# Kernel optimization log

Measured on AMD Instinct MI355X. Metric: run time of the kernel, lower is better.

Reference implementation:

```python
import jax, jax.numpy as jnp
import numpy as np

C = 768
NUM_HEADS = 12
HEAD_DIM = C // NUM_HEADS
AGENT_NUM = 49
POOL = 7  # sqrt(agent_num)
EPS = 1e-5


def _with_bias_ln(x, w, b):
    # LayerNorm over last dim, biased variance, eps=1e-5
    mu = x.mean(-1, keepdims=True)
    var = ((x - mu) ** 2).mean(-1, keepdims=True)
    return (x - mu) / jnp.sqrt(var + EPS) * w + b


def setup_inputs() -> dict:
    key = jax.random.key(0)
    ks = jax.random.split(key, 8)
    B, H, W = 8, 56, 56
    inp = {
        "x": jax.random.normal(ks[0], (B, C, H, W), dtype=jnp.float32),
        "y": jax.random.normal(ks[1], (B, C, H, W), dtype=jnp.float32),
        "ln1_w": jnp.ones((C,), jnp.float32),
        "ln1_b": jnp.zeros((C,), jnp.float32),
        "ln2_w": jnp.ones((C,), jnp.float32),
        "ln2_b": jnp.zeros((C,), jnp.float32),
        # torch nn.Linear weight layout: [out, in]
        "wq1": jax.random.normal(ks[2], (C, C), jnp.float32) * 0.02,
        "wq2": jax.random.normal(ks[3], (C, C), jnp.float32) * 0.02,
        "wkv": jax.random.normal(ks[4], (2 * C, C), jnp.float32) * 0.02,
        "wproj": jax.random.normal(ks[5], (C, C), jnp.float32) * 0.02,
        "bproj": jnp.zeros((C,), jnp.float32),
    }
    return inp


def reference(x, y, ln1_w, ln1_b, ln2_w, ln2_b, wq1, wq2, wkv, wproj, bproj):
    b, c, h, w = x.shape
    n = h * w
    nh, hd = NUM_HEADS, HEAD_DIM
    scale = hd ** (-0.5)

    # NCHW -> (b, n, c) token layout
    xt = x.reshape(b, c, n).transpose(0, 2, 1)
    yt = y.reshape(b, c, n).transpose(0, 2, 1)

    xt = _with_bias_ln(xt, ln1_w, ln1_b)
    yt = _with_bias_ln(yt, ln2_w, ln2_b)

    q = jnp.einsum('bnc,oc->bno', xt, wq1)        # (b, n, c)
    q_agent = jnp.einsum('bnc,oc->bno', yt, wq2)  # (b, n, c)
    kv = jnp.einsum('bnc,oc->bno', xt, wkv)       # (b, n, 2c)
    k, v = kv[..., :c], kv[..., c:]

    # Adaptive avg pool q_agent to 7x7 agent tokens (56/7 = 8 exact windows)
    qa = q_agent.reshape(b, h, w, c)
    qa = qa.reshape(b, POOL, h // POOL, POOL, w // POOL, c).mean(axis=(2, 4))
    agent_tokens = qa.reshape(b, AGENT_NUM, c)

    # split heads: (b, heads, tokens, head_dim)
    q = q.reshape(b, n, nh, hd).transpose(0, 2, 1, 3)
    k = k.reshape(b, n, nh, hd).transpose(0, 2, 1, 3)
    v = v.reshape(b, n, nh, hd).transpose(0, 2, 1, 3)
    at = agent_tokens.reshape(b, AGENT_NUM, nh, hd).transpose(0, 2, 1, 3)

    # stage 1: agent tokens attend over keys -> pooled values
    agent_attn = jax.nn.softmax(jnp.einsum('bhad,bhnd->bhan', at * scale, k), axis=-1)
    agent_v = jnp.einsum('bhan,bhnd->bhad', agent_attn, v)  # (b, h, A, hd)

    # stage 2: queries attend over agent tokens
    q_attn = jax.nn.softmax(jnp.einsum('bhnd,bhad->bhna', q * scale, at), axis=-1)
    out = jnp.einsum('bhna,bhad->bhnd', q_attn, agent_v)  # (b, h, n, hd)

    out = out.transpose(0, 2, 1, 3).reshape(b, n, c)
    out = jnp.einsum('bnc,oc->bno', out, wproj) + bproj
    return out.transpose(0, 2, 1).reshape(b, c, h, w)
```

## Files before the change

### kernel.cpp

```cpp
#include <hip/hip_runtime.h>

typedef unsigned short u16;
typedef u16 u16x4 __attribute__((ext_vector_type(4)));
typedef u16 u16x8 __attribute__((ext_vector_type(8)));
typedef __bf16 bf16x8 __attribute__((ext_vector_type(8)));
typedef float f32x4 __attribute__((ext_vector_type(4)));

__device__ __forceinline__ float b2f(u16 u) {
    union { unsigned int i; float f; } v; v.i = ((unsigned int)u) << 16; return v.f;
}
__device__ __forceinline__ u16 f2b(float f) {
    union { float f; unsigned int i; } v; v.f = f;
    unsigned int r = v.i + 0x7fffu + ((v.i >> 16) & 1u);
    return (u16)(r >> 16);
}
__device__ __forceinline__ void gload_lds16(const u16* g, u16* l) {
    __builtin_amdgcn_global_load_lds(
        (const __attribute__((address_space(1))) void*)g,
        (__attribute__((address_space(3))) void*)l, 16, 0, 0);
}
__device__ __forceinline__ bf16x8 ones_frag() {
    union { u16x8 u; bf16x8 b; } v;
    #pragma unroll
    for (int i = 0; i < 8; ++i) v.u[i] = 0x3F80;
    return v.b;
}
#define LGKM_BARRIER do { \
    asm volatile("s_waitcnt lgkmcnt(0)" ::: "memory"); \
    __builtin_amdgcn_s_barrier(); \
    __builtin_amdgcn_sched_barrier(0); } while (0)

__global__ __launch_bounds__(256) void pack_w_kernel(
    const float* __restrict__ wq1, const float* __restrict__ wq2,
    const float* __restrict__ wkv, const float* __restrict__ wproj,
    u16* __restrict__ wcat, u16* __restrict__ wq2b, u16* __restrict__ wpb,
    u16* __restrict__ at_a) {
    int e = blockIdx.x * 256 + threadIdx.x;
    const float scale = 0.125f;
    wcat[e]           = f2b(wq1[e] * scale);
    wcat[589824 + e]  = f2b(wkv[e] * scale);
    wcat[1179648 + e] = f2b(wkv[589824 + e]);
    wq2b[e]           = f2b(wq2[e]);
    wpb[e]            = f2b(wproj[e]);
    if (e < 92160) {
        int bb = e / 11520, rem = e - bb * 11520;
        at_a[(size_t)bb * 49152 + 37632 + rem] = 0;
    }
}

__global__ __launch_bounds__(256) void ln_x_kernel(
    const float* __restrict__ x, const float* __restrict__ lw,
    const float* __restrict__ lb, u16* __restrict__ xn) {
    __shared__ float red[16][64];
    __shared__ float red2[16][64];
    __shared__ float smu[64];
    __shared__ float srs[64];
    __shared__ u16 tl[128][68];
    const int bx = blockIdx.x;
    const int b = bx / 49, tile = bx - b * 49;
    const int pos0 = tile * 64;
    const int t = threadIdx.x;
    const int pq = t & 15, q = t >> 4;
    const float* xb = x + (size_t)b * 2408448 + pos0;

    f32x4 s = {0.f, 0.f, 0.f, 0.f}, s2 = {0.f, 0.f, 0.f, 0.f};
    #pragma unroll 8
    for (int c = q; c < 768; c += 16) {
        f32x4 v = *(const f32x4*)&xb[(size_t)c * 3136 + pq * 4];
        s += v; s2 += v * v;
    }
    *(f32x4*)&red[q][pq * 4] = s;
    *(f32x4*)&red2[q][pq * 4] = s2;
    __syncthreads();
    if (t < 64) {
        float ss = 0.f, qq = 0.f;
        #pragma unroll
        for (int r = 0; r < 16; ++r) { ss += red[r][t]; qq += red2[r][t]; }
        float mu = ss * (1.0f / 768.0f);
        float var = qq * (1.0f / 768.0f) - mu * mu;
        smu[t] = mu;
        srs[t] = rsqrtf(var + 1e-5f);
    }
    __syncthreads();

    const int p = t >> 2, sub = t & 3;
    const size_t orow = ((size_t)(b * 3136 + pos0 + p)) * 768;
    for (int c0 = 0; c0 < 768; c0 += 128) {
        #pragma unroll
        for (int s8 = 0; s8 < 8; ++s8) {
            const int cr = s8 * 16 + q;
            f32x4 v = *(const f32x4*)&xb[(size_t)(c0 + cr) * 3136 + pq * 4];
            u16x4 pk;
            pk[0] = f2b(v[0]); pk[1] = f2b(v[1]); pk[2] = f2b(v[2]); pk[3] = f2b(v[3]);
            *(u16x4*)&tl[cr][pq * 4] = pk;
        }
        __syncthreads();
        const float mu = smu[p], rs = srs[p];
        #pragma unroll
        for (int k = 0; k < 4; ++k) {
            const int cb = k * 32 + sub * 8;
            f32x4 w0 = *(const f32x4*)&lw[c0 + cb];
            f32x4 w1 = *(const f32x4*)&lw[c0 + cb + 4];
            f32x4 b0 = *(const f32x4*)&lb[c0 + cb];
            f32x4 b1 = *(const f32x4*)&lb[c0 + cb + 4];
            u16x8 o;
            #pragma unroll
            for (int j = 0; j < 4; ++j) {
                float v = b2f(tl[cb + j][p]);
                o[j] = f2b((v - mu) * rs * w0[j] + b0[j]);
            }
            #pragma unroll
            for (int j = 0; j < 4; ++j) {
                float v = b2f(tl[cb + 4 + j][p]);
                o[4 + j] = f2b((v - mu) * rs * w1[j] + b1[j]);
            }
            *(u16x8*)&xn[orow + c0 + cb] = o;
        }
        __syncthreads();
    }
}

__global__ __launch_bounds__(256) void y_stats_kernel(
    const float* __restrict__ y, float* __restrict__ rsb, float* __restrict__ mrsb) {
    __shared__ float red[16][64];
    __shared__ float red2[16][64];
    const int bx = blockIdx.x;
    const int b = bx / 49, tile = bx - b * 49;
    const int pos0 = tile * 64;
    const int t = threadIdx.x, pq = t & 15, q = t >> 4;
    const float* yb = y + (size_t)b * 2408448 + pos0;
    f32x4 s = {0.f, 0.f, 0.f, 0.f}, s2 = {0.f, 0.f, 0.f, 0.f};
    #pragma unroll 8
    for (int c = q; c < 768; c += 16) {
        f32x4 v = *(const f32x4*)&yb[(size_t)c * 3136 + pq * 4];
        s += v; s2 += v * v;
    }
    *(f32x4*)&red[q][pq * 4] = s;
    *(f32x4*)&red2[q][pq * 4] = s2;
    __syncthreads();
    if (t < 64) {
        float ss = 0.f, qq = 0.f;
        #pragma unroll
        for (int r = 0; r < 16; ++r) { ss += red[r][t]; qq += red2[r][t]; }
        float mu = ss * (1.0f / 768.0f);
        float var = qq * (1.0f / 768.0f) - mu * mu;
        float rv = rsqrtf(var + 1e-5f);
        rsb[(size_t)b * 3136 + pos0 + t] = rv;
        mrsb[(size_t)b * 3136 + pos0 + t] = mu * rv;
    }
}

__global__ __launch_bounds__(256) void y_pool_kernel(
    const float* __restrict__ y, const float* __restrict__ lw,
    const float* __restrict__ lb, const float* __restrict__ rsb,
    const float* __restrict__ mrsb, u16* __restrict__ at_a) {
    const int cgrp = blockIdx.x;
    const int bpi  = blockIdx.y;
    const int b = bpi / 7, pi = bpi - b * 7;
    const int t = threadIdx.x, lane = t & 63, w = t >> 6;
    const int pbase = b * 3136 + pi * 448;
    const int p0 = (lane >> 3) * 56 + (lane & 7);
    float rsv[7], s3f[7];
    #pragma unroll
    for (int it = 0; it < 7; ++it) {
        rsv[it] = rsb[pbase + p0 + it * 8];
        float m = mrsb[pbase + p0 + it * 8];
        #pragma unroll
        for (int msk = 1; msk < 64; msk <<= 1) m += __shfl_xor(m, msk, 64);
        s3f[it] = m;
    }
    const float* yb = y + (size_t)b * 2408448 + pi * 448 + p0;
    u16* yo = at_a + ((size_t)b * 64 + pi * 7) * 768;
    for (int ci = 0; ci < 16; ++ci) {
        const int c = cgrp * 64 + w * 16 + ci;
        const float* yc = yb + (size_t)c * 3136;
        float v[7];
        #pragma unroll
        for (int it = 0; it < 7; ++it) v[it] = yc[it * 8] * rsv[it];
        #pragma unroll
        for (int it = 0; it < 7; ++it) {
            float s = v[it];
            #pragma unroll
            for (int msk = 1; msk < 64; msk <<= 1) s += __shfl_xor(s, msk, 64);
            v[it] = s;
        }
        if (lane == 0) {
            const float wv = lw[c], bv = lb[c];
            #pragma unroll
            for (int it = 0; it < 7; ++it)
                yo[(size_t)it * 768 + c] = f2b(wv * (v[it] - s3f[it]) * (1.0f / 64.0f) + bv);
        }
    }
}

template<int MODE, int NCT>
__global__ __launch_bounds__(256) void gemm_bt_kernel(
    const u16* __restrict__ A, const u16* __restrict__ B,
    u16* __restrict__ qk, u16* __restrict__ vT,
    float* __restrict__ Cf, const float* __restrict__ bias) {
    __shared__ u16 As[128 * 64];
    __shared__ u16 Bs[128 * 64];
    const int t = threadIdx.x;
    const int lane = t & 63;
    const int w = t >> 6;
    const int wr = w >> 1, wc = w & 1;
    const int l15 = lane & 15, l4 = lane >> 4;

    const int nwg = gridDim.x;
    const int orig = blockIdx.x;
    const int xcd = orig & 7;
    const int qd = nwg >> 3, r = nwg & 7;
    const int wg = (xcd < r ? xcd * (qd + 1) : r * (qd + 1) + (xcd - r) * qd) + (orig >> 3);
    const int ct = wg % NCT, rt = wg / NCT;

    const u16* Ab = A + (size_t)rt * 128 * 768;
    const u16* Bb = B + (size_t)ct * 128 * 768;
    const int grh = lane >> 3;
    const int gsl = (lane & 7) ^ grh;

    f32x4 acc[4][4];
    #pragma unroll
    for (int mi = 0; mi < 4; ++mi)
        #pragma unroll
        for (int ni = 0; ni < 4; ++ni)
            acc[mi][ni] = (f32x4){0.f, 0.f, 0.f, 0.f};

    for (int kt = 0; kt < 12; ++kt) {
        if (kt) __syncthreads();
        #pragma unroll
        for (int i = 0; i < 4; ++i) {
            const int chunk = w * 4 + i;
            const int row = chunk * 8 + grh;
            gload_lds16(Ab + (size_t)row * 768 + kt * 64 + gsl * 8, &As[chunk * 512]);
            gload_lds16(Bb + (size_t)row * 768 + kt * 64 + gsl * 8, &Bs[chunk * 512]);
        }
        __syncthreads();
        #pragma unroll
        for (int ks = 0; ks < 2; ++ks) {
            bf16x8 af[4], bfv[4];
            #pragma unroll
            for (int mi = 0; mi < 4; ++mi) {
                const int row = wr * 64 + mi * 16 + l15;
                af[mi] = *(const bf16x8*)&As[row * 64 + (((ks * 4 + l4) ^ (row & 7)) * 8)];
            }
            #pragma unroll
            for (int ni = 0; ni < 4; ++ni) {
                const int row = wc * 64 + ni * 16 + l15;
                bfv[ni] = *(const bf16x8*)&Bs[row * 64 + (((ks * 4 + l4) ^ (row & 7)) * 8)];
            }
            #pragma unroll
            for (int mi = 0; mi < 4; ++mi)
                #pragma unroll
                for (int ni = 0; ni < 4; ++ni)
                    acc[mi][ni] = __builtin_amdgcn_mfma_f32_16x16x32_bf16(
                        af[mi], bfv[ni], acc[mi][ni], 0, 0, 0);
        }
    }

    if constexpr (MODE == 0) {
        #pragma unroll
        for (int mi = 0; mi < 4; ++mi)
            #pragma unroll
            for (int ni = 0; ni < 4; ++ni) {
                const int row0 = rt * 128 + wr * 64 + mi * 16 + l4 * 4;
                const int col = ct * 128 + wc * 64 + ni * 16 + l15;
                if (col < 1536) {
                    #pragma unroll
                    for (int rr = 0; rr < 4; ++rr)
                        qk[(size_t)(row0 + rr) * 1536 + col] = f2b(acc[mi][ni][rr]);
                } else {
                    const int c = col - 1536;
                    const int bb = row0 / 3136;
                    const int nn2 = row0 - bb * 3136;
                    u16x4 pk;
                    #pragma unroll
                    for (int rr = 0; rr < 4; ++rr) pk[rr] = f2b(acc[mi][ni][rr]);
                    *(u16x4*)&vT[((size_t)(bb * 768 + c)) * 3136 + nn2] = pk;
                }
            }
    } else if constexpr (MODE == 1) {
        #pragma unroll
        for (int ni = 0; ni < 4; ++ni) {
            const int col = ct * 128 + wc * 64 + ni * 16 + l15;
            const float bv = bias[col];
            #pragma unroll
            for (int mi = 0; mi < 4; ++mi) {
                const int grow = rt * 128 + wr * 64 + mi * 16 + l4 * 4;
                const int bb = grow / 3136;
                const int nn2 = grow - bb * 3136;
                f32x4 vv = acc[mi][ni];
                vv[0] += bv; vv[1] += bv; vv[2] += bv; vv[3] += bv;
                *(f32x4*)(Cf + (size_t)bb * 2408448 + (size_t)col * 3136 + nn2) = vv;
            }
        }
    } else {
        #pragma unroll
        for (int mi = 0; mi < 4; ++mi)
            #pragma unroll
            for (int ni = 0; ni < 4; ++ni) {
                const int row0 = rt * 128 + wr * 64 + mi * 16 + l4 * 4;
                const int col = ct * 128 + wc * 64 + ni * 16 + l15;
                #pragma unroll
                for (int rr = 0; rr < 4; ++rr)
                    qk[(size_t)(row0 + rr) * 768 + col] = f2b(acc[mi][ni][rr]);
            }
    }
}

__global__ __launch_bounds__(256) void agent_attn_kernel(
    const u16* __restrict__ at_bf, const u16* __restrict__ qk,
    const u16* __restrict__ vT, float* __restrict__ ps,
    float* __restrict__ pav_t) {
    __shared__ u16 k_lds[2][64 * 64];
    __shared__ u16 vt_lds[2][64 * 64];
    __shared__ u16 p_lds[64 * 64];
    const int ns = blockIdx.x;
    const int bh = blockIdx.y;
    const int b = bh / 12, h = bh - b * 12;
    const int t = threadIdx.x, lane = t & 63, w = t >> 6;
    const int l15 = lane & 15, l4 = lane >> 4;

    bf16x8 atf[2];
    #pragma unroll
    for (int ks = 0; ks < 2; ++ks)
        atf[ks] = *(const bf16x8*)&at_bf[((size_t)b * 64 + 16 * w + l15) * 768 + h * 64 + ks * 32 + l4 * 8];
    const bf16x8 onef = ones_frag();

    f32x4 acc_o[4], acc_den[4];
    #pragma unroll
    for (int mi = 0; mi < 4; ++mi) {
        acc_o[mi] = (f32x4){0.f, 0.f, 0.f, 0.f};
        acc_den[mi] = (f32x4){0.f, 0.f, 0.f, 0.f};
    }

    auto STAGE = [&](int buf, int tile) {
        const int n0 = ns * 448 + tile * 64;
        #pragma unroll
        for (int p = 0; p < 2; ++p) {
            const int row = p * 32 + w * 8 + (lane >> 3);
            const int sc = ((lane & 7) ^ (row & 7)) * 8;
            gload_lds16(qk + ((size_t)(b * 3136 + n0 + row)) * 1536 + 768 + h * 64 + sc,
                        &k_lds[buf][(p * 32 + w * 8) * 64]);
            gload_lds16(vT + ((size_t)(bh * 64 + row)) * 3136 + n0 + sc,
                        &vt_lds[buf][(p * 32 + w * 8) * 64]);
        }
    };

    STAGE(0, 0);
    for (int tile = 0; tile < 7; ++tile) {
        const int buf = tile & 1;
        __syncthreads();
        if (tile < 6) STAGE(buf ^ 1, tile + 1);
        f32x4 acc_s[4];
        #pragma unroll
        for (int mi = 0; mi < 4; ++mi) acc_s[mi] = (f32x4){0.f, 0.f, 0.f, 0.f};
        #pragma unroll
        for (int ks = 0; ks < 2; ++ks)
            #pragma unroll
            for (int mi = 0; mi < 4; ++mi) {
                const int row = 16 * mi + l15;
                bf16x8 kf = *(const bf16x8*)&k_lds[buf][row * 64 + (((ks * 4 + l4) ^ (row & 7)) * 8)];
                acc_s[mi] = __builtin_amdgcn_mfma_f32_16x16x32_bf16(kf, atf[ks], acc_s[mi], 0, 0, 0);
            }
        const int a_w = 16 * w + l15;
        #pragma unroll
        for (int mi = 0; mi < 4; ++mi) {
            u16x4 pk;
            #pragma unroll
            for (int rr = 0; rr < 4; ++rr) pk[rr] = f2b(__expf(acc_s[mi][rr]));
            const int pp = (2 * mi + (l4 >> 1)) ^ (a_w & 7);
            *(u16x4*)((char*)p_lds + a_w * 128 + pp * 16 + (l4 & 1) * 8) = pk;
        }
        LGKM_BARRIER;
        #pragma unroll
        for (int ks = 0; ks < 2; ++ks) {
            const int d = 16 * w + l15;
            bf16x8 vf = *(const bf16x8*)&vt_lds[buf][d * 64 + (((ks * 4 + l4) ^ (d & 7)) * 8)];
            #pragma unroll
            for (int mi = 0; mi < 4; ++mi) {
                const int a = 16 * mi + l15;
                bf16x8 pf = *(const bf16x8*)((char*)p_lds + a * 128 + (((ks * 4 + l4) ^ (a & 7)) * 16));
                acc_o[mi] = __builtin_amdgcn_mfma_f32_16x16x32_bf16(pf, vf, acc_o[mi], 0, 0, 0);
                acc_den[mi] = __builtin_amdgcn_mfma_f32_16x16x32_bf16(onef, pf, acc_den[mi], 0, 0, 0);
            }
        }
    }
    const size_t pbase = (size_t)bh * 7 + ns;
    if (w == 0 && lane < 16) {
        #pragma unroll
        for (int mi = 0; mi < 4; ++mi)
            ps[pbase * 64 + 16 * mi + lane] = acc_den[mi][0];
    }
    #pragma unroll
    for (int mi = 0; mi < 4; ++mi)
        *(f32x4*)&pav_t[(pbase * 64 + 16 * w + l15) * 64 + 16 * mi + l4 * 4] = acc_o[mi];
}

__global__ __launch_bounds__(256) void combine_kernel(
    const float* __restrict__ ps, const float* __restrict__ pav_t,
    u16* __restrict__ av_t) {
    __shared__ float sinv[64];
    const int bh = blockIdx.x;
    const int t = threadIdx.x;
    if (t < 64) {
        float s = 0.f;
        #pragma unroll
        for (int ns = 0; ns < 7; ++ns) s += ps[((size_t)bh * 7 + ns) * 64 + t];
        sinv[t] = 1.0f / s;
    }
    __syncthreads();
    const int d = t >> 2, aseg = t & 3;
    f32x4 acc[4];
    #pragma unroll
    for (int g = 0; g < 4; ++g) acc[g] = (f32x4){0.f, 0.f, 0.f, 0.f};
    #pragma unroll
    for (int ns = 0; ns < 7; ++ns) {
        const float* src = pav_t + (((size_t)bh * 7 + ns) * 64 + d) * 64 + aseg * 16;
        #pragma unroll
        for (int g = 0; g < 4; ++g) acc[g] += *(const f32x4*)&src[g * 4];
    }
    u16x8 o0, o1;
    #pragma unroll
    for (int g = 0; g < 4; ++g)
        #pragma unroll
        for (int j = 0; j < 4; ++j) {
            const u16 v = f2b(acc[g][j] * sinv[aseg * 16 + g * 4 + j]);
            if (g < 2) o0[g * 4 + j] = v; else o1[(g - 2) * 4 + j] = v;
        }
    u16* dst = av_t + ((size_t)bh * 64 + d) * 64 + aseg * 16;
    *(u16x8*)dst = o0;
    *(u16x8*)(dst + 8) = o1;
}

__global__ __launch_bounds__(256) void q_attn_kernel(
    const u16* __restrict__ at_bf, const u16* __restrict__ qk,
    const u16* __restrict__ av_t, u16* __restrict__ attn_out) {
    __shared__ u16 q_lds[2][64 * 64];
    __shared__ u16 p_lds[64 * 64];
    const int grp = blockIdx.x;
    const int bh = blockIdx.y;
    const int b = bh / 12, h = bh - b * 12;
    const int t = threadIdx.x, lane = t & 63, w = t >> 6;
    const int l15 = lane & 15, l4 = lane >> 4;

    bf16x8 atf[4][2], avf[4][2];
    #pragma unroll
    for (int mi = 0; mi < 4; ++mi)
        #pragma unroll
        for (int ks = 0; ks < 2; ++ks) {
            atf[mi][ks] = *(const bf16x8*)&at_bf[((size_t)b * 64 + 16 * mi + l15) * 768 + h * 64 + ks * 32 + l4 * 8];
            avf[mi][ks] = *(const bf16x8*)&av_t[((size_t)bh * 64 + 16 * mi + l15) * 64 + ks * 32 + l4 * 8];
        }
    const bf16x8 onef = ones_frag();

    auto STAGE_Q = [&](int buf, int nt) {
        const int n0 = nt * 64;
        #pragma unroll
        for (int p = 0; p < 2; ++p) {
            const int row = p * 32 + w * 8 + (lane >> 3);
            const int sc = ((lane & 7) ^ (row & 7)) * 8;
            gload_lds16(qk + ((size_t)(b * 3136 + n0 + row)) * 1536 + h * 64 + sc,
                        &q_lds[buf][(p * 32 + w * 8) * 64]);
        }
    };

    STAGE_Q(0, grp * 7);
    const int nn = 16 * w + l15;
    for (int i = 0; i < 7; ++i) {
        const int buf = i & 1;
        const int nt = grp * 7 + i;
        __syncthreads();
        if (i < 6) STAGE_Q(buf ^ 1, nt + 1);
        f32x4 acc_l[4];
        #pragma unroll
        for (int mi = 0; mi < 4; ++mi) acc_l[mi] = (f32x4){0.f, 0.f, 0.f, 0.f};
        #pragma unroll
        for (int ks = 0; ks < 2; ++ks) {
            bf16x8 qf = *(const bf16x8*)&q_lds[buf][nn * 64 + (((ks * 4 + l4) ^ (nn & 7)) * 8)];
            #pragma unroll
            for (int mi = 0; mi < 4; ++mi)
                acc_l[mi] = __builtin_amdgcn_mfma_f32_16x16x32_bf16(atf[mi][ks], qf, acc_l[mi], 0, 0, 0);
        }
        #pragma unroll
        for (int mi = 0; mi < 4; ++mi) {
            u16x4 pk;
            #pragma unroll
            for (int rr = 0; rr < 4; ++rr) {
                const int a = 16 * mi + l4 * 4 + rr;
                pk[rr] = (a < 49) ? f2b(__expf(acc_l[mi][rr])) : (u16)0;
            }
            const int pp = (2 * mi + (l4 >> 1)) ^ (nn & 7);
            *(u16x4*)((char*)p_lds + nn * 128 + pp * 16 + (l4 & 1) * 8) = pk;
        }
        LGKM_BARRIER;
        f32x4 acc_o[4], den;
        #pragma unroll
        for (int mi = 0; mi < 4; ++mi) acc_o[mi] = (f32x4){0.f, 0.f, 0.f, 0.f};
        den = (f32x4){0.f, 0.f, 0.f, 0.f};
        #pragma unroll
        for (int ks = 0; ks < 2; ++ks) {
            bf16x8 pf = *(const bf16x8*)((char*)p_lds + nn * 128 + (((ks * 4 + l4) ^ (nn & 7)) * 16));
            den = __builtin_amdgcn_mfma_f32_16x16x32_bf16(onef, pf, den, 0, 0, 0);
            #pragma unroll
            for (int mi = 0; mi < 4; ++mi)
                acc_o[mi] = __builtin_amdgcn_mfma_f32_16x16x32_bf16(avf[mi][ks], pf, acc_o[mi], 0, 0, 0);
        }
        const float rinv = 1.0f / den[0];
        const size_t obase = ((size_t)(b * 3136 + nt * 64 + nn)) * 768 + h * 64;
        #pragma unroll
        for (int mi = 0; mi < 4; ++mi) {
            u16x4 ov;
            #pragma unroll
            for (int rr = 0; rr < 4; ++rr) ov[rr] = f2b(acc_o[mi][rr] * rinv);
            *(u16x4*)&attn_out[obase + 16 * mi + l4 * 4] = ov;
        }
    }
}

extern "C" void kernel_launch(void* const* d_in, const int* in_sizes, int n_in,
                              void* d_out, int out_size, void* d_ws, size_t ws_size,
                              hipStream_t stream) {
    (void)in_sizes; (void)n_in; (void)out_size; (void)ws_size;
    const float* x     = (const float*)d_in[0];
    const float* y     = (const float*)d_in[1];
    const float* ln1w  = (const float*)d_in[2];
    const float* ln1b  = (const float*)d_in[3];
    const float* ln2w  = (const float*)d_in[4];
    const float* ln2b  = (const float*)d_in[5];
    const float* wq1   = (const float*)d_in[6];
    const float* wq2   = (const float*)d_in[7];
    const float* wkv   = (const float*)d_in[8];
    const float* wproj = (const float*)d_in[9];
    const float* bproj = (const float*)d_in[10];
    float* out = (float*)d_out;

    char* ws = (char*)d_ws;
    u16*   xn     = (u16*)(ws);
    u16*   qk     = (u16*)(ws + 38535168);
    u16*   vT     = (u16*)(ws + 115605504);
    u16*   wcat   = (u16*)(ws + 154140672);
    u16*   wq2b   = (u16*)(ws + 157679616);
    u16*   wpb    = (u16*)(ws + 158859264);
    u16*   at_a   = (u16*)(ws + 160038912);
    u16*   at_bf  = (u16*)(ws + 160825344);
    float* ps     = (float*)(ws + 161611776);
    float* rsb    = (float*)(ws + 161783808);
    float* mrsb   = (float*)(ws + 161884160);
    u16*   av_t   = (u16*)(ws + 161984512);
    float* pav_t  = (float*)(ws);
    u16*   attn_out = xn;

    pack_w_kernel<<<dim3(2304), dim3(256), 0, stream>>>(wq1, wq2, wkv, wproj, wcat, wq2b, wpb, at_a);
    ln_x_kernel<<<dim3(392), dim3(256), 0, stream>>>(x, ln1w, ln1b, xn);
    y_stats_kernel<<<dim3(392), dim3(256), 0, stream>>>(y, rsb, mrsb);
    y_pool_kernel<<<dim3(12, 56), dim3(256), 0, stream>>>(y, ln2w, ln2b, rsb, mrsb, at_a);
    gemm_bt_kernel<0, 18><<<dim3(3528), dim3(256), 0, stream>>>(xn, wcat, qk, vT, nullptr, nullptr);
    gemm_bt_kernel<2, 6><<<dim3(24), dim3(256), 0, stream>>>(at_a, wq2b, at_bf, nullptr, nullptr, nullptr);
    agent_attn_kernel<<<dim3(7, 96), dim3(256), 0, stream>>>(at_bf, qk, vT, ps, pav_t);
    combine_kernel<<<dim3(96), dim3(256), 0, stream>>>(ps, pav_t, av_t);
    q_attn_kernel<<<dim3(7, 96), dim3(256), 0, stream>>>(at_bf, qk, av_t, attn_out);
    gemm_bt_kernel<1, 6><<<dim3(1176), dim3(256), 0, stream>>>(attn_out, wpb, nullptr, nullptr, out, bproj);
}
```

Baseline: 319.5 us.

## Use 256x256 double-buffered GEMM tiles for QKV and projection GEMMs

Replaces the 128x128 single-buffered GEMM with a 256x256 tile, 512-thread kernel that double-buffers LDS and prefetches the next K-tile while computing the current one. It uses explicit vmcnt waits, barriers and setprio around the MFMA bursts. The goal is more reuse per loaded byte and hiding global load latency in the large QKV and projection GEMMs. The small agent-token GEMM moves to a separate 128-tile kernel. The cost is 128KB of LDS per block, which lowers occupancy, and fewer workgroups for the projection GEMM (294 blocks).

```diff
diff --git a/kernel.cpp b/kernel.cpp
--- a/kernel.cpp
+++ b/kernel.cpp
@@ -194,16 +194,17 @@
 }
 
 template<int MODE, int NCT>
-__global__ __launch_bounds__(256) void gemm_bt_kernel(
+__global__ __launch_bounds__(512, 2) void gemm256_kernel(
     const u16* __restrict__ A, const u16* __restrict__ B,
     u16* __restrict__ qk, u16* __restrict__ vT,
     float* __restrict__ Cf, const float* __restrict__ bias) {
-    __shared__ u16 As[128 * 64];
-    __shared__ u16 Bs[128 * 64];
+    __shared__ u16 As[2][256 * 64];
+    __shared__ u16 Bs[2][256 * 64];
     const int t = threadIdx.x;
     const int lane = t & 63;
     const int w = t >> 6;
-    const int wr = w >> 1, wc = w & 1;
+    const int wr = w >> 2;
+    const int wc = w & 3;
     const int l15 = lane & 15, l4 = lane >> 4;
 
     const int nwg = gridDim.x;
@@ -213,57 +214,80 @@
     const int wg = (xcd < r ? xcd * (qd + 1) : r * (qd + 1) + (xcd - r) * qd) + (orig >> 3);
     const int ct = wg % NCT, rt = wg / NCT;
 
-    const u16* Ab = A + (size_t)rt * 128 * 768;
-    const u16* Bb = B + (size_t)ct * 128 * 768;
-    const int grh = lane >> 3;
-    const int gsl = (lane & 7) ^ grh;
-
-    f32x4 acc[4][4];
-    #pragma unroll
-    for (int mi = 0; mi < 4; ++mi)
+    const u16* Ab = A + (size_t)rt * 256 * 768;
+    const u16* Bb = B + (size_t)ct * 256 * 768;
+    const int gsl = (lane & 7) ^ (lane >> 3);
+
+    f32x4 acc[8][4];
+    #pragma unroll
+    for (int mi = 0; mi < 8; ++mi)
         #pragma unroll
         for (int ni = 0; ni < 4; ++ni)
             acc[mi][ni] = (f32x4){0.f, 0.f, 0.f, 0.f};
 
+    auto ISSUE = [&](int buf, int kt) {
+        const size_t go = (size_t)(w * 8 + (lane >> 3)) * 768 + (size_t)kt * 64 + gsl * 8;
+        #pragma unroll
+        for (int i = 0; i < 4; ++i) {
+            gload_lds16(Ab + go + (size_t)i * 49152, &As[buf][(i * 64 + w * 8) * 64]);
+            gload_lds16(Bb + go + (size_t)i * 49152, &Bs[buf][(i * 64 + w * 8) * 64]);
+        }
+    };
+
+    ISSUE(0, 0);
     for (int kt = 0; kt < 12; ++kt) {
-        if (kt) __syncthreads();
-        #pragma unroll
-        for (int i = 0; i < 4; ++i) {
-            const int chunk = w * 4 + i;
-            const int row = chunk * 8 + grh;
-            gload_lds16(Ab + (size_t)row * 768 + kt * 64 + gsl * 8, &As[chunk * 512]);
-            gload_lds16(Bb + (size_t)row * 768 + kt * 64 + gsl * 8, &Bs[chunk * 512]);
-        }
-        __syncthreads();
-        #pragma unroll
-        for (int ks = 0; ks < 2; ++ks) {
-            bf16x8 af[4], bfv[4];
-            #pragma unroll
-            for (int mi = 0; mi < 4; ++mi) {
-                const int row = wr * 64 + mi * 16 + l15;
-                af[mi] = *(const bf16x8*)&As[row * 64 + (((ks * 4 + l4) ^ (row & 7)) * 8)];
-            }
+        const int buf = kt & 1;
+        if (kt < 11) {
+            ISSUE(buf ^ 1, kt + 1);
+            asm volatile("s_waitcnt vmcnt(8)" ::: "memory");
+        } else {
+            asm volatile("s_waitcnt vmcnt(0)" ::: "memory");
+        }
+        __builtin_amdgcn_sched_barrier(0);
+        __builtin_amdgcn_s_barrier();
+        __builtin_amdgcn_sched_barrier(0);
+        const u16* as_ = &As[buf][0];
+        const u16* bs_ = &Bs[buf][0];
+        #pragma unroll
+        for (int p = 0; p < 4; ++p) {
+            const int mh = p >> 1, nh = p & 1;
+            bf16x8 af[4][2], bfv[2][2];
+            #pragma unroll
+            for (int ks = 0; ks < 2; ++ks) {
+                const int sw = ((ks * 4 + l4) ^ (l15 & 7)) * 8;
+                #pragma unroll
+                for (int mi = 0; mi < 4; ++mi)
+                    af[mi][ks] = *(const bf16x8*)&as_[(wr * 128 + mh * 64 + mi * 16 + l15) * 64 + sw];
+                #pragma unroll
+                for (int ni = 0; ni < 2; ++ni)
+                    bfv[ni][ks] = *(const bf16x8*)&bs_[(wc * 64 + nh * 32 + ni * 16 + l15) * 64 + sw];
+            }
+            __builtin_amdgcn_s_barrier();
+            asm volatile("s_waitcnt lgkmcnt(0)" ::: "memory");
+            __builtin_amdgcn_sched_barrier(0);
+            __builtin_amdgcn_s_setprio(1);
+            #pragma unroll
+            for (int ks = 0; ks < 2; ++ks)
+                #pragma unroll
+                for (int mi = 0; mi < 4; ++mi)
+                    #pragma unroll
+                    for (int ni = 0; ni < 2; ++ni)
+                        acc[mh * 4 + mi][nh * 2 + ni] = __builtin_amdgcn_mfma_f32_16x16x32_bf16(
+                            af[mi][ks], bfv[ni][ks], acc[mh * 4 + mi][nh * 2 + ni], 0, 0, 0);
+            __builtin_amdgcn_s_setprio(0);
+            __builtin_amdgcn_sched_barrier(0);
+            __builtin_amdgcn_s_barrier();
+            __builtin_amdgcn_sched_barrier(0);
+        }
+    }
+
+    if constexpr (MODE == 0) {
+        #pragma unroll
+        for (int mi = 0; mi < 8; ++mi)
             #pragma unroll
             for (int ni = 0; ni < 4; ++ni) {
-                const int row = wc * 64 + ni * 16 + l15;
-                bfv[ni] = *(const bf16x8*)&Bs[row * 64 + (((ks * 4 + l4) ^ (row & 7)) * 8)];
-            }
-            #pragma unroll
-            for (int mi = 0; mi < 4; ++mi)
-                #pragma unroll
-                for (int ni = 0; ni < 4; ++ni)
-                    acc[mi][ni] = __builtin_amdgcn_mfma_f32_16x16x32_bf16(
-                        af[mi], bfv[ni], acc[mi][ni], 0, 0, 0);
-        }
-    }
-
-    if constexpr (MODE == 0) {
-        #pragma unroll
-        for (int mi = 0; mi < 4; ++mi)
-            #pragma unroll
-            for (int ni = 0; ni < 4; ++ni) {
-                const int row0 = rt * 128 + wr * 64 + mi * 16 + l4 * 4;
-                const int col = ct * 128 + wc * 64 + ni * 16 + l15;
+                const int row0 = rt * 256 + wr * 128 + mi * 16 + l4 * 4;
+                const int col = ct * 256 + wc * 64 + ni * 16 + l15;
                 if (col < 1536) {
                     #pragma unroll
                     for (int rr = 0; rr < 4; ++rr)
@@ -278,14 +302,14 @@
                     *(u16x4*)&vT[((size_t)(bb * 768 + c)) * 3136 + nn2] = pk;
                 }
             }
-    } else if constexpr (MODE == 1) {
+    } else {
         #pragma unroll
         for (int ni = 0; ni < 4; ++ni) {
-            const int col = ct * 128 + wc * 64 + ni * 16 + l15;
+            const int col = ct * 256 + wc * 64 + ni * 16 + l15;
             const float bv = bias[col];
             #pragma unroll
-            for (int mi = 0; mi < 4; ++mi) {
-                const int grow = rt * 128 + wr * 64 + mi * 16 + l4 * 4;
+            for (int mi = 0; mi < 8; ++mi) {
+                const int grow = rt * 256 + wr * 128 + mi * 16 + l4 * 4;
                 const int bb = grow / 3136;
                 const int nn2 = grow - bb * 3136;
                 f32x4 vv = acc[mi][ni];
@@ -293,18 +317,74 @@
                 *(f32x4*)(Cf + (size_t)bb * 2408448 + (size_t)col * 3136 + nn2) = vv;
             }
         }
-    } else {
-        #pragma unroll
-        for (int mi = 0; mi < 4; ++mi)
+    }
+}
+
+template<int NCT>
+__global__ __launch_bounds__(256) void gemm128_kernel(
+    const u16* __restrict__ A, const u16* __restrict__ B, u16* __restrict__ C) {
+    __shared__ u16 As[128 * 64];
+    __shared__ u16 Bs[128 * 64];
+    const int t = threadIdx.x;
+    const int lane = t & 63;
+    const int w = t >> 6;
+    const int wr = w >> 1, wc = w & 1;
+    const int l15 = lane & 15, l4 = lane >> 4;
+    const int ct = blockIdx.x % NCT, rt = blockIdx.x / NCT;
+
+    const u16* Ab = A + (size_t)rt * 128 * 768;
+    const u16* Bb = B + (size_t)ct * 128 * 768;
+    const int grh = lane >> 3;
+    const int gsl = (lane & 7) ^ grh;
+
+    f32x4 acc[4][4];
+    #pragma unroll
+    for (int mi = 0; mi < 4; ++mi)
+        #pragma unroll
+        for (int ni = 0; ni < 4; ++ni)
+            acc[mi][ni] = (f32x4){0.f, 0.f, 0.f, 0.f};
+
+    for (int kt = 0; kt < 12; ++kt) {
+        if (kt) __syncthreads();
+        #pragma unroll
+        for (int i = 0; i < 4; ++i) {
+            const int chunk = w * 4 + i;
+            const int row = chunk * 8 + grh;
+            gload_lds16(Ab + (size_t)row * 768 + kt * 64 + gsl * 8, &As[chunk * 512]);
+            gload_lds16(Bb + (size_t)row * 768 + kt * 64 + gsl * 8, &Bs[chunk * 512]);
+        }
+        __syncthreads();
+        #pragma unroll
+        for (int ks = 0; ks < 2; ++ks) {
+            bf16x8 af[4], bfv[4];
+            #pragma unroll
+            for (int mi = 0; mi < 4; ++mi) {
+                const int row = wr * 64 + mi * 16 + l15;
+                af[mi] = *(const bf16x8*)&As[row * 64 + (((ks * 4 + l4) ^ (row & 7)) * 8)];
+            }
             #pragma unroll
             for (int ni = 0; ni < 4; ++ni) {
-                const int row0 = rt * 128 + wr * 64 + mi * 16 + l4 * 4;
-                const int col = ct * 128 + wc * 64 + ni * 16 + l15;
+                const int row = wc * 64 + ni * 16 + l15;
+                bfv[ni] = *(const bf16x8*)&Bs[row * 64 + (((ks * 4 + l4) ^ (row & 7)) * 8)];
+            }
+            #pragma unroll
+            for (int mi = 0; mi < 4; ++mi)
                 #pragma unroll
-                for (int rr = 0; rr < 4; ++rr)
-                    qk[(size_t)(row0 + rr) * 768 + col] = f2b(acc[mi][ni][rr]);
-            }
-    }
+                for (int ni = 0; ni < 4; ++ni)
+                    acc[mi][ni] = __builtin_amdgcn_mfma_f32_16x16x32_bf16(
+                        af[mi], bfv[ni], acc[mi][ni], 0, 0, 0);
+        }
+    }
+    #pragma unroll
+    for (int mi = 0; mi < 4; ++mi)
+        #pragma unroll
+        for (int ni = 0; ni < 4; ++ni) {
+            const int row0 = rt * 128 + wr * 64 + mi * 16 + l4 * 4;
+            const int col = ct * 128 + wc * 64 + ni * 16 + l15;
+            #pragma unroll
+            for (int rr = 0; rr < 4; ++rr)
+                C[(size_t)(row0 + rr) * 768 + col] = f2b(acc[mi][ni][rr]);
+        }
 }
 
 __global__ __launch_bounds__(256) void agent_attn_kernel(
@@ -554,10 +634,10 @@
     ln_x_kernel<<<dim3(392), dim3(256), 0, stream>>>(x, ln1w, ln1b, xn);
     y_stats_kernel<<<dim3(392), dim3(256), 0, stream>>>(y, rsb, mrsb);
     y_pool_kernel<<<dim3(12, 56), dim3(256), 0, stream>>>(y, ln2w, ln2b, rsb, mrsb, at_a);
-    gemm_bt_kernel<0, 18><<<dim3(3528), dim3(256), 0, stream>>>(xn, wcat, qk, vT, nullptr, nullptr);
-    gemm_bt_kernel<2, 6><<<dim3(24), dim3(256), 0, stream>>>(at_a, wq2b, at_bf, nullptr, nullptr, nullptr);
+    gemm256_kernel<0, 9><<<dim3(882), dim3(512), 0, stream>>>(xn, wcat, qk, vT, nullptr, nullptr);
+    gemm128_kernel<6><<<dim3(24), dim3(256), 0, stream>>>(at_a, wq2b, at_bf);
     agent_attn_kernel<<<dim3(7, 96), dim3(256), 0, stream>>>(at_bf, qk, vT, ps, pav_t);
     combine_kernel<<<dim3(96), dim3(256), 0, stream>>>(ps, pav_t, av_t);
     q_attn_kernel<<<dim3(7, 96), dim3(256), 0, stream>>>(at_bf, qk, av_t, attn_out);
-    gemm_bt_kernel<1, 6><<<dim3(1176), dim3(256), 0, stream>>>(attn_out, wpb, nullptr, nullptr, out, bproj);
-}
+    gemm256_kernel<1, 3><<<dim3(294), dim3(512), 0, stream>>>(attn_out, wpb, nullptr, nullptr, out, bproj);
+}
```

Result: slower. 393.6 us (+23.2%).

## Merge launches: fuse pack+stats, norm+pool, QKV+agent GEMMs, combine into q_attn

Applied to the files above, without the earlier changes.

Reduces the launch count from ten to six. Weight packing is merged with the x/y LayerNorm statistics, x normalization (now split into two channel halves) is merged with y pooling, and the agent-token GEMM runs inside the QKV GEMM grid. The combine step is folded into q_attn, which rebuilds av_t in LDS in every block. GEMM tiles are also remapped into groups of 4 row tiles for L2 reuse. The cost is that the combine work is repeated 7 times per head and x is read twice (once for stats, once for normalization), but launch gaps and some serialization go away.

```diff
diff --git a/kernel.cpp b/kernel.cpp
--- a/kernel.cpp
+++ b/kernel.cpp
@@ -30,43 +30,43 @@
     __builtin_amdgcn_s_barrier(); \
     __builtin_amdgcn_sched_barrier(0); } while (0)
 
-__global__ __launch_bounds__(256) void pack_w_kernel(
+__global__ __launch_bounds__(256) void pack_stats_kernel(
     const float* __restrict__ wq1, const float* __restrict__ wq2,
     const float* __restrict__ wkv, const float* __restrict__ wproj,
     u16* __restrict__ wcat, u16* __restrict__ wq2b, u16* __restrict__ wpb,
-    u16* __restrict__ at_a) {
-    int e = blockIdx.x * 256 + threadIdx.x;
-    const float scale = 0.125f;
-    wcat[e]           = f2b(wq1[e] * scale);
-    wcat[589824 + e]  = f2b(wkv[e] * scale);
-    wcat[1179648 + e] = f2b(wkv[589824 + e]);
-    wq2b[e]           = f2b(wq2[e]);
-    wpb[e]            = f2b(wproj[e]);
-    if (e < 92160) {
-        int bb = e / 11520, rem = e - bb * 11520;
-        at_a[(size_t)bb * 49152 + 37632 + rem] = 0;
-    }
-}
-
-__global__ __launch_bounds__(256) void ln_x_kernel(
-    const float* __restrict__ x, const float* __restrict__ lw,
-    const float* __restrict__ lb, u16* __restrict__ xn) {
+    u16* __restrict__ at_a,
+    const float* __restrict__ x, const float* __restrict__ y,
+    float* __restrict__ xmu, float* __restrict__ xrs,
+    float* __restrict__ rsb, float* __restrict__ mrsb) {
     __shared__ float red[16][64];
     __shared__ float red2[16][64];
-    __shared__ float smu[64];
-    __shared__ float srs[64];
-    __shared__ u16 tl[128][68];
-    const int bx = blockIdx.x;
+    const int bxg = blockIdx.x;
+    const int t = threadIdx.x;
+    if (bxg < 2304) {
+        const int e = bxg * 256 + t;
+        const float scale = 0.125f;
+        wcat[e]           = f2b(wq1[e] * scale);
+        wcat[589824 + e]  = f2b(wkv[e] * scale);
+        wcat[1179648 + e] = f2b(wkv[589824 + e]);
+        wq2b[e]           = f2b(wq2[e]);
+        wpb[e]            = f2b(wproj[e]);
+        if (e < 92160) {
+            int bb = e / 11520, rem = e - bb * 11520;
+            at_a[(size_t)bb * 49152 + 37632 + rem] = 0;
+        }
+        return;
+    }
+    const int bx0 = bxg - 2304;
+    const int isY = bx0 >= 392;
+    const int bx = isY ? bx0 - 392 : bx0;
     const int b = bx / 49, tile = bx - b * 49;
     const int pos0 = tile * 64;
-    const int t = threadIdx.x;
     const int pq = t & 15, q = t >> 4;
-    const float* xb = x + (size_t)b * 2408448 + pos0;
-
+    const float* src = (isY ? y : x) + (size_t)b * 2408448 + pos0;
     f32x4 s = {0.f, 0.f, 0.f, 0.f}, s2 = {0.f, 0.f, 0.f, 0.f};
     #pragma unroll 8
     for (int c = q; c < 768; c += 16) {
-        f32x4 v = *(const f32x4*)&xb[(size_t)c * 3136 + pq * 4];
+        f32x4 v = *(const f32x4*)&src[(size_t)c * 3136 + pq * 4];
         s += v; s2 += v * v;
     }
     *(f32x4*)&red[q][pq * 4] = s;
@@ -78,86 +78,74 @@
         for (int r = 0; r < 16; ++r) { ss += red[r][t]; qq += red2[r][t]; }
         float mu = ss * (1.0f / 768.0f);
         float var = qq * (1.0f / 768.0f) - mu * mu;
-        smu[t] = mu;
-        srs[t] = rsqrtf(var + 1e-5f);
-    }
-    __syncthreads();
-
-    const int p = t >> 2, sub = t & 3;
-    const size_t orow = ((size_t)(b * 3136 + pos0 + p)) * 768;
-    for (int c0 = 0; c0 < 768; c0 += 128) {
-        #pragma unroll
-        for (int s8 = 0; s8 < 8; ++s8) {
-            const int cr = s8 * 16 + q;
-            f32x4 v = *(const f32x4*)&xb[(size_t)(c0 + cr) * 3136 + pq * 4];
-            u16x4 pk;
-            pk[0] = f2b(v[0]); pk[1] = f2b(v[1]); pk[2] = f2b(v[2]); pk[3] = f2b(v[3]);
-            *(u16x4*)&tl[cr][pq * 4] = pk;
-        }
-        __syncthreads();
-        const float mu = smu[p], rs = srs[p];
-        #pragma unroll
-        for (int k = 0; k < 4; ++k) {
-            const int cb = k * 32 + sub * 8;
-            f32x4 w0 = *(const f32x4*)&lw[c0 + cb];
-            f32x4 w1 = *(const f32x4*)&lw[c0 + cb + 4];
-            f32x4 b0 = *(const f32x4*)&lb[c0 + cb];
-            f32x4 b1 = *(const f32x4*)&lb[c0 + cb + 4];
-            u16x8 o;
-            #pragma unroll
-            for (int j = 0; j < 4; ++j) {
-                float v = b2f(tl[cb + j][p]);
-                o[j] = f2b((v - mu) * rs * w0[j] + b0[j]);
-            }
-            #pragma unroll
-            for (int j = 0; j < 4; ++j) {
-                float v = b2f(tl[cb + 4 + j][p]);
-                o[4 + j] = f2b((v - mu) * rs * w1[j] + b1[j]);
-            }
-            *(u16x8*)&xn[orow + c0 + cb] = o;
-        }
-        __syncthreads();
-    }
-}
-
-__global__ __launch_bounds__(256) void y_stats_kernel(
-    const float* __restrict__ y, float* __restrict__ rsb, float* __restrict__ mrsb) {
-    __shared__ float red[16][64];
-    __shared__ float red2[16][64];
-    const int bx = blockIdx.x;
-    const int b = bx / 49, tile = bx - b * 49;
-    const int pos0 = tile * 64;
-    const int t = threadIdx.x, pq = t & 15, q = t >> 4;
-    const float* yb = y + (size_t)b * 2408448 + pos0;
-    f32x4 s = {0.f, 0.f, 0.f, 0.f}, s2 = {0.f, 0.f, 0.f, 0.f};
-    #pragma unroll 8
-    for (int c = q; c < 768; c += 16) {
-        f32x4 v = *(const f32x4*)&yb[(size_t)c * 3136 + pq * 4];
-        s += v; s2 += v * v;
-    }
-    *(f32x4*)&red[q][pq * 4] = s;
-    *(f32x4*)&red2[q][pq * 4] = s2;
-    __syncthreads();
-    if (t < 64) {
-        float ss = 0.f, qq = 0.f;
-        #pragma unroll
-        for (int r = 0; r < 16; ++r) { ss += red[r][t]; qq += red2[r][t]; }
-        float mu = ss * (1.0f / 768.0f);
-        float var = qq * (1.0f / 768.0f) - mu * mu;
         float rv = rsqrtf(var + 1e-5f);
-        rsb[(size_t)b * 3136 + pos0 + t] = rv;
-        mrsb[(size_t)b * 3136 + pos0 + t] = mu * rv;
-    }
-}
-
-__global__ __launch_bounds__(256) void y_pool_kernel(
-    const float* __restrict__ y, const float* __restrict__ lw,
-    const float* __restrict__ lb, const float* __restrict__ rsb,
+        const size_t o = (size_t)b * 3136 + pos0 + t;
+        if (isY) { rsb[o] = rv; mrsb[o] = mu * rv; }
+        else     { xmu[o] = mu; xrs[o] = rv; }
+    }
+}
+
+__global__ __launch_bounds__(256) void norm_pool_kernel(
+    const float* __restrict__ x, const float* __restrict__ lw1,
+    const float* __restrict__ lb1, const float* __restrict__ xmu,
+    const float* __restrict__ xrs, u16* __restrict__ xn,
+    const float* __restrict__ y, const float* __restrict__ lw2,
+    const float* __restrict__ lb2, const float* __restrict__ rsb,
     const float* __restrict__ mrsb, u16* __restrict__ at_a) {
-    const int cgrp = blockIdx.x;
-    const int bpi  = blockIdx.y;
+    __shared__ u16 tl[128][68];
+    const int bxg = blockIdx.x;
+    const int t = threadIdx.x;
+    if (bxg < 784) {
+        const int half = bxg / 392;
+        const int bx = bxg - half * 392;
+        const int b = bx / 49, tile = bx - b * 49;
+        const int pos0 = tile * 64;
+        const int pq = t & 15, q = t >> 4;
+        const int p = t >> 2, sub = t & 3;
+        const float* xb = x + (size_t)b * 2408448 + pos0;
+        const float mu = xmu[(size_t)b * 3136 + pos0 + p];
+        const float rs = xrs[(size_t)b * 3136 + pos0 + p];
+        const size_t orow = ((size_t)(b * 3136 + pos0 + p)) * 768;
+        for (int ci = 0; ci < 3; ++ci) {
+            const int c0 = half * 384 + ci * 128;
+            #pragma unroll
+            for (int s8 = 0; s8 < 8; ++s8) {
+                const int cr = s8 * 16 + q;
+                f32x4 v = *(const f32x4*)&xb[(size_t)(c0 + cr) * 3136 + pq * 4];
+                u16x4 pk;
+                pk[0] = f2b(v[0]); pk[1] = f2b(v[1]); pk[2] = f2b(v[2]); pk[3] = f2b(v[3]);
+                *(u16x4*)&tl[cr][pq * 4] = pk;
+            }
+            __syncthreads();
+            #pragma unroll
+            for (int k = 0; k < 4; ++k) {
+                const int cb = k * 32 + sub * 8;
+                f32x4 w0 = *(const f32x4*)&lw1[c0 + cb];
+                f32x4 w1 = *(const f32x4*)&lw1[c0 + cb + 4];
+                f32x4 b0 = *(const f32x4*)&lb1[c0 + cb];
+                f32x4 b1 = *(const f32x4*)&lb1[c0 + cb + 4];
+                u16x8 o;
+                #pragma unroll
+                for (int j = 0; j < 4; ++j) {
+                    float v = b2f(tl[cb + j][p]);
+                    o[j] = f2b((v - mu) * rs * w0[j] + b0[j]);
+                }
+                #pragma unroll
+                for (int j = 0; j < 4; ++j) {
+                    float v = b2f(tl[cb + 4 + j][p]);
+                    o[4 + j] = f2b((v - mu) * rs * w1[j] + b1[j]);
+                }
+                *(u16x8*)&xn[orow + c0 + cb] = o;
+            }
+            __syncthreads();
+        }
+        return;
+    }
+    const int j = bxg - 784;
+    const int cgrp = j % 12;
+    const int bpi = j / 12;
     const int b = bpi / 7, pi = bpi - b * 7;
-    const int t = threadIdx.x, lane = t & 63, w = t >> 6;
+    const int lane = t & 63, w = t >> 6;
     const int pbase = b * 3136 + pi * 448;
     const int p0 = (lane >> 3) * 56 + (lane & 7);
     float rsv[7], s3f[7];
@@ -185,7 +173,7 @@
             v[it] = s;
         }
         if (lane == 0) {
-            const float wv = lw[c], bv = lb[c];
+            const float wv = lw2[c], bv = lb2[c];
             #pragma unroll
             for (int it = 0; it < 7; ++it)
                 yo[(size_t)it * 768 + c] = f2b(wv * (v[it] - s3f[it]) * (1.0f / 64.0f) + bv);
@@ -193,25 +181,17 @@
     }
 }
 
-template<int MODE, int NCT>
-__global__ __launch_bounds__(256) void gemm_bt_kernel(
-    const u16* __restrict__ A, const u16* __restrict__ B,
+template<int MODE>
+__device__ __forceinline__ void gemm_body(
+    int rt, int ct, const u16* __restrict__ A, const u16* __restrict__ B,
     u16* __restrict__ qk, u16* __restrict__ vT,
-    float* __restrict__ Cf, const float* __restrict__ bias) {
-    __shared__ u16 As[128 * 64];
-    __shared__ u16 Bs[128 * 64];
+    float* __restrict__ Cf, const float* __restrict__ bias,
+    u16* As, u16* Bs) {
     const int t = threadIdx.x;
     const int lane = t & 63;
     const int w = t >> 6;
     const int wr = w >> 1, wc = w & 1;
     const int l15 = lane & 15, l4 = lane >> 4;
-
-    const int nwg = gridDim.x;
-    const int orig = blockIdx.x;
-    const int xcd = orig & 7;
-    const int qd = nwg >> 3, r = nwg & 7;
-    const int wg = (xcd < r ? xcd * (qd + 1) : r * (qd + 1) + (xcd - r) * qd) + (orig >> 3);
-    const int ct = wg % NCT, rt = wg / NCT;
 
     const u16* Ab = A + (size_t)rt * 128 * 768;
     const u16* Bb = B + (size_t)ct * 128 * 768;
@@ -307,6 +287,45 @@
     }
 }
 
+__device__ __forceinline__ void map_tile(int orig, int nwg, int NCT,
+                                         int& rt, int& ct) {
+    const int xcd = orig & 7;
+    const int qd = nwg >> 3, r = nwg & 7;
+    const int wg = (xcd < r ? xcd * (qd + 1) : r * (qd + 1) + (xcd - r) * qd) + (orig >> 3);
+    const int grp = NCT * 4;
+    const int rtg = wg / grp, rem = wg % grp;
+    ct = rem >> 2;
+    rt = rtg * 4 + (rem & 3);
+}
+
+__global__ __launch_bounds__(256) void gemm_qkv_at_kernel(
+    const u16* __restrict__ xn, const u16* __restrict__ wcat,
+    u16* __restrict__ qk, u16* __restrict__ vT,
+    const u16* __restrict__ at_a, const u16* __restrict__ wq2b,
+    u16* __restrict__ at_bf) {
+    __shared__ u16 As[128 * 64];
+    __shared__ u16 Bs[128 * 64];
+    const int bx = blockIdx.x;
+    if (bx < 3528) {
+        int rt, ct;
+        map_tile(bx, 3528, 18, rt, ct);
+        gemm_body<0>(rt, ct, xn, wcat, qk, vT, nullptr, nullptr, As, Bs);
+    } else {
+        const int wg = bx - 3528;
+        gemm_body<2>(wg / 6, wg % 6, at_a, wq2b, at_bf, nullptr, nullptr, nullptr, As, Bs);
+    }
+}
+
+__global__ __launch_bounds__(256) void gemm_proj_kernel(
+    const u16* __restrict__ attn_out, const u16* __restrict__ wpb,
+    float* __restrict__ out, const float* __restrict__ bproj) {
+    __shared__ u16 As[128 * 64];
+    __shared__ u16 Bs[128 * 64];
+    int rt, ct;
+    map_tile(blockIdx.x, 1176, 6, rt, ct);
+    gemm_body<1>(rt, ct, attn_out, wpb, nullptr, nullptr, out, bproj, As, Bs);
+}
+
 __global__ __launch_bounds__(256) void agent_attn_kernel(
     const u16* __restrict__ at_bf, const u16* __restrict__ qk,
     const u16* __restrict__ vT, float* __restrict__ ps,
@@ -396,63 +415,20 @@
         *(f32x4*)&pav_t[(pbase * 64 + 16 * w + l15) * 64 + 16 * mi + l4 * 4] = acc_o[mi];
 }
 
-__global__ __launch_bounds__(256) void combine_kernel(
-    const float* __restrict__ ps, const float* __restrict__ pav_t,
-    u16* __restrict__ av_t) {
-    __shared__ float sinv[64];
-    const int bh = blockIdx.x;
-    const int t = threadIdx.x;
-    if (t < 64) {
-        float s = 0.f;
-        #pragma unroll
-        for (int ns = 0; ns < 7; ++ns) s += ps[((size_t)bh * 7 + ns) * 64 + t];
-        sinv[t] = 1.0f / s;
-    }
-    __syncthreads();
-    const int d = t >> 2, aseg = t & 3;
-    f32x4 acc[4];
-    #pragma unroll
-    for (int g = 0; g < 4; ++g) acc[g] = (f32x4){0.f, 0.f, 0.f, 0.f};
-    #pragma unroll
-    for (int ns = 0; ns < 7; ++ns) {
-        const float* src = pav_t + (((size_t)bh * 7 + ns) * 64 + d) * 64 + aseg * 16;
-        #pragma unroll
-        for (int g = 0; g < 4; ++g) acc[g] += *(const f32x4*)&src[g * 4];
-    }
-    u16x8 o0, o1;
-    #pragma unroll
-    for (int g = 0; g < 4; ++g)
-        #pragma unroll
-        for (int j = 0; j < 4; ++j) {
-            const u16 v = f2b(acc[g][j] * sinv[aseg * 16 + g * 4 + j]);
-            if (g < 2) o0[g * 4 + j] = v; else o1[(g - 2) * 4 + j] = v;
-        }
-    u16* dst = av_t + ((size_t)bh * 64 + d) * 64 + aseg * 16;
-    *(u16x8*)dst = o0;
-    *(u16x8*)(dst + 8) = o1;
-}
-
 __global__ __launch_bounds__(256) void q_attn_kernel(
     const u16* __restrict__ at_bf, const u16* __restrict__ qk,
-    const u16* __restrict__ av_t, u16* __restrict__ attn_out) {
+    const float* __restrict__ ps, const float* __restrict__ pav_t,
+    u16* __restrict__ attn_out) {
     __shared__ u16 q_lds[2][64 * 64];
     __shared__ u16 p_lds[64 * 64];
+    __shared__ u16 av_lds[64 * 64];
+    __shared__ float sinv[64];
     const int grp = blockIdx.x;
     const int bh = blockIdx.y;
     const int b = bh / 12, h = bh - b * 12;
     const int t = threadIdx.x, lane = t & 63, w = t >> 6;
     const int l15 = lane & 15, l4 = lane >> 4;
 
-    bf16x8 atf[4][2], avf[4][2];
-    #pragma unroll
-    for (int mi = 0; mi < 4; ++mi)
-        #pragma unroll
-        for (int ks = 0; ks < 2; ++ks) {
-            atf[mi][ks] = *(const bf16x8*)&at_bf[((size_t)b * 64 + 16 * mi + l15) * 768 + h * 64 + ks * 32 + l4 * 8];
-            avf[mi][ks] = *(const bf16x8*)&av_t[((size_t)bh * 64 + 16 * mi + l15) * 64 + ks * 32 + l4 * 8];
-        }
-    const bf16x8 onef = ones_frag();
-
     auto STAGE_Q = [&](int buf, int nt) {
         const int n0 = nt * 64;
         #pragma unroll
@@ -463,8 +439,49 @@
                         &q_lds[buf][(p * 32 + w * 8) * 64]);
         }
     };
-
     STAGE_Q(0, grp * 7);
+
+    if (t < 64) {
+        float s = 0.f;
+        #pragma unroll
+        for (int ns = 0; ns < 7; ++ns) s += ps[((size_t)bh * 7 + ns) * 64 + t];
+        sinv[t] = 1.0f / s;
+    }
+    __syncthreads();
+    {
+        const int d = t >> 2, aseg = t & 3;
+        f32x4 acc[4];
+        #pragma unroll
+        for (int g = 0; g < 4; ++g) acc[g] = (f32x4){0.f, 0.f, 0.f, 0.f};
+        #pragma unroll
+        for (int ns = 0; ns < 7; ++ns) {
+            const float* src = pav_t + (((size_t)bh * 7 + ns) * 64 + d) * 64 + aseg * 16;
+            #pragma unroll
+            for (int g = 0; g < 4; ++g) acc[g] += *(const f32x4*)&src[g * 4];
+        }
+        u16x8 o0, o1;
+        #pragma unroll
+        for (int g = 0; g < 4; ++g)
+            #pragma unroll
+            for (int jj = 0; jj < 4; ++jj) {
+                const u16 v = f2b(acc[g][jj] * sinv[aseg * 16 + g * 4 + jj]);
+                if (g < 2) o0[g * 4 + jj] = v; else o1[(g - 2) * 4 + jj] = v;
+            }
+        *(u16x8*)&av_lds[d * 64 + aseg * 16] = o0;
+        *(u16x8*)&av_lds[d * 64 + aseg * 16 + 8] = o1;
+    }
+    __syncthreads();
+
+    bf16x8 atf[4][2], avf[4][2];
+    #pragma unroll
+    for (int mi = 0; mi < 4; ++mi)
+        #pragma unroll
+        for (int ks = 0; ks < 2; ++ks) {
+            atf[mi][ks] = *(const bf16x8*)&at_bf[((size_t)b * 64 + 16 * mi + l15) * 768 + h * 64 + ks * 32 + l4 * 8];
+            avf[mi][ks] = *(const bf16x8*)&av_lds[(16 * mi + l15) * 64 + ks * 32 + l4 * 8];
+        }
+    const bf16x8 onef = ones_frag();
+
     const int nn = 16 * w + l15;
     for (int i = 0; i < 7; ++i) {
         const int buf = i & 1;
@@ -546,18 +563,18 @@
     float* ps     = (float*)(ws + 161611776);
     float* rsb    = (float*)(ws + 161783808);
     float* mrsb   = (float*)(ws + 161884160);
-    u16*   av_t   = (u16*)(ws + 161984512);
+    float* xmu    = (float*)(ws + 161984512);
+    float* xrs    = (float*)(ws + 162084864);
     float* pav_t  = (float*)(ws);
-    u16*   attn_out = xn;
-
-    pack_w_kernel<<<dim3(2304), dim3(256), 0, stream>>>(wq1, wq2, wkv, wproj, wcat, wq2b, wpb, at_a);
-    ln_x_kernel<<<dim3(392), dim3(256), 0, stream>>>(x, ln1w, ln1b, xn);
-    y_stats_kernel<<<dim3(392), dim3(256), 0, stream>>>(y, rsb, mrsb);
-    y_pool_kernel<<<dim3(12, 56), dim3(256), 0, stream>>>(y, ln2w, ln2b, rsb, mrsb, at_a);
-    gemm_bt_kernel<0, 18><<<dim3(3528), dim3(256), 0, stream>>>(xn, wcat, qk, vT, nullptr, nullptr);
-    gemm_bt_kernel<2, 6><<<dim3(24), dim3(256), 0, stream>>>(at_a, wq2b, at_bf, nullptr, nullptr, nullptr);
+    u16*   attn_out = vT;
+
+    pack_stats_kernel<<<dim3(3088), dim3(256), 0, stream>>>(
+        wq1, wq2, wkv, wproj, wcat, wq2b, wpb, at_a, x, y, xmu, xrs, rsb, mrsb);
+    norm_pool_kernel<<<dim3(1456), dim3(256), 0, stream>>>(
+        x, ln1w, ln1b, xmu, xrs, xn, y, ln2w, ln2b, rsb, mrsb, at_a);
+    gemm_qkv_at_kernel<<<dim3(3552), dim3(256), 0, stream>>>(
+        xn, wcat, qk, vT, at_a, wq2b, at_bf);
     agent_attn_kernel<<<dim3(7, 96), dim3(256), 0, stream>>>(at_bf, qk, vT, ps, pav_t);
-    combine_kernel<<<dim3(96), dim3(256), 0, stream>>>(ps, pav_t, av_t);
-    q_attn_kernel<<<dim3(7, 96), dim3(256), 0, stream>>>(at_bf, qk, av_t, attn_out);
-    gemm_bt_kernel<1, 6><<<dim3(1176), dim3(256), 0, stream>>>(attn_out, wpb, nullptr, nullptr, out, bproj);
-}
+    q_attn_kernel<<<dim3(7, 96), dim3(256), 0, stream>>>(at_bf, qk, ps, pav_t, attn_out);
+    gemm_proj_kernel<<<dim3(1176), dim3(256), 0, stream>>>(attn_out, wpb, out, bproj);
+}
```

New measurement: 303.2 us (median of 4 runs). 1.05x faster.
